# Optimization experiments

Hardware: AMD Instinct MI355X
Metric: run time of the kernel (lower is better)

## Reference

```python
import jax, jax.numpy as jnp
import numpy as np

B_BATCH = 128
IN_F = 1024
OUT_F = 1024
CODE = 2
FACTOR = 1.0


def setup_inputs() -> dict:
    key = jax.random.key(0)
    k = jax.random.split(key, 7)
    bound = 1.0 / np.sqrt(IN_F)
    return {
        "input": jax.random.normal(k[0], (B_BATCH, IN_F), dtype=jnp.float32),
        "codes": jax.random.normal(k[1], (B_BATCH, CODE, CODE), dtype=jnp.float32),
        "weight": jax.random.uniform(k[2], (IN_F, OUT_F), minval=-bound, maxval=bound, dtype=jnp.float32),
        "A": jax.random.uniform(k[3], (IN_F, CODE), minval=-bound, maxval=bound, dtype=jnp.float32),
        "B": jax.random.uniform(k[4], (CODE, OUT_F), minval=-bound, maxval=bound, dtype=jnp.float32),
        "bias": jax.random.uniform(k[5], (OUT_F,), minval=-bound, maxval=bound, dtype=jnp.float32),
        "bias_context": jax.random.uniform(k[6], (CODE, OUT_F), minval=-bound, maxval=bound, dtype=jnp.float32),
    }


def reference(input, codes, weight, A, B, bias, bias_context):
    # per-sample low-rank modulation: A [in,code] x codes [b,code,code] -> [b,in,code]
    w = jnp.einsum('ir,brp->bip', A, codes)
    # [b,in,code] x B [code,out] -> [b,in,out]
    context_weights = jnp.einsum('bir,rj->bij', w, B)
    # diag(codes) [b,code] @ bias_context [code,out] -> [b,out]
    context_bias = jnp.diagonal(codes, axis1=-2, axis2=-1) @ bias_context
    combined_weight = weight + FACTOR * context_weights  # [b,in,out]
    combined_bias = bias + FACTOR * context_bias          # [b,out]
    return jnp.einsum('bi,bij->bj', input, combined_weight) + combined_bias
```

## Files before the change

### kernel.cpp

```cpp
#include <hip/hip_runtime.h>

#define N_BATCH 128
#define IN_F 1024
#define OUT_F 1024
#define BT 8
#define JT 32
#define SEG 32
#define RSTRIDE 36
#define SSTRIDE 292

__global__ __launch_bounds__(256) void geps_one(
    const float* __restrict__ input,
    const float* __restrict__ codes,
    const float* __restrict__ weight,
    const float* __restrict__ A,
    const float* __restrict__ Bm,
    const float* __restrict__ bias,
    const float* __restrict__ bctx,
    float* __restrict__ out)
{
    __shared__ __align__(16) float s[SEG * SSTRIDE];
    __shared__ float s_u[BT][2];
    __shared__ float s_v[BT][4];

    const int t = threadIdx.x;
    const int j0 = blockIdx.x * JT;
    const int b0 = blockIdx.y * BT;

    #pragma unroll
    for (int it = 0; it < 8; ++it) {
        const int F = t + 256 * it;
        const int r = F >> 8;
        const int i4 = F & 255;
        const int ks = i4 >> 3, g = i4 & 7;
        const float4 val = ((const float4*)input)[(size_t)(b0 + r) * (IN_F / 4) + i4];
        *(float4*)&s[ks * SSTRIDE + r * RSTRIDE + 4 * g] = val;
    }
    __syncthreads();

    {
        const int grp = t >> 4, l = t & 15;
        const int row = grp >> 1, rr = grp & 1;
        float p = 0.f;
        #pragma unroll 4
        for (int ii = 0; ii < 64; ++ii) {
            const int i = l + 16 * ii;
            const float x = s[(i >> 5) * SSTRIDE + row * RSTRIDE + (i & 31)];
            p = fmaf(x, A[2 * i + rr], p);
        }
        #pragma unroll
        for (int off = 8; off > 0; off >>= 1)
            p += __shfl_down(p, off, 16);
        if (l == 0) s_u[row][rr] = p;
    }
    __syncthreads();

    if (t < BT) {
        const int b = b0 + t;
        const float u0 = s_u[t][0], u1 = s_u[t][1];
        const float c00 = codes[b * 4 + 0], c01 = codes[b * 4 + 1];
        const float c10 = codes[b * 4 + 2], c11 = codes[b * 4 + 3];
        s_v[t][0] = fmaf(u0, c00, u1 * c10);
        s_v[t][1] = fmaf(u0, c01, u1 * c11);
        s_v[t][2] = c00;
        s_v[t][3] = c11;
    }

    const int jg = t & 7, ks = t >> 3;
    const int col4 = (j0 >> 2) + jg;
    const float4* W4 = (const float4*)weight;
    const float* segbase = &s[ks * SSTRIDE];

    float4 acc[BT];
    #pragma unroll
    for (int r = 0; r < BT; ++r) acc[r] = make_float4(0.f, 0.f, 0.f, 0.f);

    #pragma unroll
    for (int g = 0; g < 8; ++g) {
        float4 a[BT];
        #pragma unroll
        for (int r = 0; r < BT; ++r)
            a[r] = *(const float4*)&segbase[r * RSTRIDE + 4 * g];
        #pragma unroll
        for (int q = 0; q < 4; ++q) {
            const float4 w = W4[(size_t)(ks * 32 + 4 * g + q) * (OUT_F / 4) + col4];
            #pragma unroll
            for (int r = 0; r < BT; ++r) {
                const float av = (q == 0) ? a[r].x : (q == 1) ? a[r].y
                               : (q == 2) ? a[r].z : a[r].w;
                acc[r].x = fmaf(av, w.x, acc[r].x);
                acc[r].y = fmaf(av, w.y, acc[r].y);
                acc[r].z = fmaf(av, w.z, acc[r].z);
                acc[r].w = fmaf(av, w.w, acc[r].w);
            }
        }
    }
    __syncthreads();

    #pragma unroll
    for (int r = 0; r < BT; ++r)
        *(float4*)&s[ks * SSTRIDE + r * RSTRIDE + 4 * jg] = acc[r];
    __syncthreads();

    {
        const int row = t >> 5, col = t & 31;
        float sum = 0.f;
        #pragma unroll
        for (int k = 0; k < SEG; ++k)
            sum += s[k * SSTRIDE + row * RSTRIDE + col];

        const int j = j0 + col;
        const int b = b0 + row;
        const float v0 = s_v[row][0], v1 = s_v[row][1];
        const float c00 = s_v[row][2], c11 = s_v[row][3];
        out[(size_t)b * OUT_F + j] = sum
            + v0 * Bm[j] + v1 * Bm[OUT_F + j]
            + bias[j]
            + c00 * bctx[j] + c11 * bctx[OUT_F + j];
    }
}

extern "C" void kernel_launch(void* const* d_in, const int* in_sizes, int n_in,
                              void* d_out, int out_size, void* d_ws, size_t ws_size,
                              hipStream_t stream) {
    const float* input = (const float*)d_in[0];
    const float* codes = (const float*)d_in[1];
    const float* weight = (const float*)d_in[2];
    const float* A = (const float*)d_in[3];
    const float* Bm = (const float*)d_in[4];
    const float* bias = (const float*)d_in[5];
    const float* bctx = (const float*)d_in[6];
    float* out = (float*)d_out;

    dim3 grid(OUT_F / JT, N_BATCH / BT);
    dim3 block(256);
    geps_one<<<grid, block, 0, stream>>>(input, codes, weight, A, Bm, bias, bctx, out);
}
```

Measured before the change: 77.35 us.

## Software-pipeline weight and LDS loads, hoist epilogue loads, vectorize A reduction

All global loads (input tile, bias/Bm/bctx columns, codes) are issued up front so their latency overlaps. The u = x·A reduction now uses float4 loads of A and x with one 32-lane reduction computing both rank components. The main weight loop double-buffers weight rows two groups ahead and shared-memory activations one group ahead, and launch_bounds is set to request 2 blocks per CU. This aims to hide global and LDS latency in a bandwidth-bound GEMV-like kernel, at the cost of more registers and a risk of spills under the occupancy hint.

```diff
diff --git a/kernel.cpp b/kernel.cpp
--- a/kernel.cpp
+++ b/kernel.cpp
@@ -9,7 +9,7 @@
 #define RSTRIDE 36
 #define SSTRIDE 292
 
-__global__ __launch_bounds__(256) void geps_one(
+__global__ __launch_bounds__(256, 2) void geps_two(
     const float* __restrict__ input,
     const float* __restrict__ codes,
     const float* __restrict__ weight,
@@ -27,39 +27,65 @@
     const int j0 = blockIdx.x * JT;
     const int b0 = blockIdx.y * BT;
 
+    float4 stg[8];
+    #pragma unroll
+    for (int it = 0; it < 8; ++it) {
+        const int F = t + 256 * it;
+        const int r = F >> 8;
+        const int i4 = F & 255;
+        stg[it] = ((const float4*)input)[(size_t)(b0 + r) * (IN_F / 4) + i4];
+    }
+
+    const int jcol = j0 + (t & 31);
+    const float bm0 = Bm[jcol];
+    const float bm1 = Bm[OUT_F + jcol];
+    const float bj  = bias[jcol];
+    const float bq0 = bctx[jcol];
+    const float bq1 = bctx[OUT_F + jcol];
+
+    float c00 = 0.f, c01 = 0.f, c10 = 0.f, c11 = 0.f;
+    if (t < BT) {
+        const int b = b0 + t;
+        c00 = codes[b * 4 + 0]; c01 = codes[b * 4 + 1];
+        c10 = codes[b * 4 + 2]; c11 = codes[b * 4 + 3];
+    }
+
     #pragma unroll
     for (int it = 0; it < 8; ++it) {
         const int F = t + 256 * it;
         const int r = F >> 8;
         const int i4 = F & 255;
         const int ks = i4 >> 3, g = i4 & 7;
-        const float4 val = ((const float4*)input)[(size_t)(b0 + r) * (IN_F / 4) + i4];
-        *(float4*)&s[ks * SSTRIDE + r * RSTRIDE + 4 * g] = val;
+        *(float4*)&s[ks * SSTRIDE + r * RSTRIDE + 4 * g] = stg[it];
     }
     __syncthreads();
 
     {
-        const int grp = t >> 4, l = t & 15;
-        const int row = grp >> 1, rr = grp & 1;
-        float p = 0.f;
-        #pragma unroll 4
-        for (int ii = 0; ii < 64; ++ii) {
-            const int i = l + 16 * ii;
-            const float x = s[(i >> 5) * SSTRIDE + row * RSTRIDE + (i & 31)];
-            p = fmaf(x, A[2 * i + rr], p);
+        const int row = t >> 5, l = t & 31;
+        float u0 = 0.f, u1 = 0.f;
+        #pragma unroll
+        for (int ii = 0; ii < 8; ++ii) {
+            const int i4 = l + 32 * ii;
+            const int ks = i4 >> 3, g = i4 & 7;
+            const float4 x  = *(const float4*)&s[ks * SSTRIDE + row * RSTRIDE + 4 * g];
+            const float4 A0 = ((const float4*)A)[2 * i4];
+            const float4 A1 = ((const float4*)A)[2 * i4 + 1];
+            u0 = fmaf(x.x, A0.x, u0); u1 = fmaf(x.x, A0.y, u1);
+            u0 = fmaf(x.y, A0.z, u0); u1 = fmaf(x.y, A0.w, u1);
+            u0 = fmaf(x.z, A1.x, u0); u1 = fmaf(x.z, A1.y, u1);
+            u0 = fmaf(x.w, A1.z, u0); u1 = fmaf(x.w, A1.w, u1);
         }
         #pragma unroll
-        for (int off = 8; off > 0; off >>= 1)
-            p += __shfl_down(p, off, 16);
-        if (l == 0) s_u[row][rr] = p;
+        for (int off = 16; off > 0; off >>= 1) {
+            u0 += __shfl_down(u0, off, 32);
+            u1 += __shfl_down(u1, off, 32);
+        }
+        if (l == 0) { s_u[row][0] = u0; s_u[row][1] = u1; }
     }
     __syncthreads();
 
     if (t < BT) {
-        const int b = b0 + t;
         const float u0 = s_u[t][0], u1 = s_u[t][1];
-        const float c00 = codes[b * 4 + 0], c01 = codes[b * 4 + 1];
-        const float c10 = codes[b * 4 + 2], c11 = codes[b * 4 + 3];
         s_v[t][0] = fmaf(u0, c00, u1 * c10);
         s_v[t][1] = fmaf(u0, c01, u1 * c11);
         s_v[t][2] = c00;
@@ -68,31 +94,52 @@
 
     const int jg = t & 7, ks = t >> 3;
     const int col4 = (j0 >> 2) + jg;
-    const float4* W4 = (const float4*)weight;
+    const float4* Wc = (const float4*)weight + col4;
     const float* segbase = &s[ks * SSTRIDE];
 
     float4 acc[BT];
     #pragma unroll
     for (int r = 0; r < BT; ++r) acc[r] = make_float4(0.f, 0.f, 0.f, 0.f);
 
+    float4 w0[4], w1[4], aC[BT];
+    #pragma unroll
+    for (int q = 0; q < 4; ++q) w0[q] = Wc[(size_t)(ks * 32 + q) * (OUT_F / 4)];
+    #pragma unroll
+    for (int q = 0; q < 4; ++q) w1[q] = Wc[(size_t)(ks * 32 + 4 + q) * (OUT_F / 4)];
+    #pragma unroll
+    for (int r = 0; r < BT; ++r) aC[r] = *(const float4*)&segbase[r * RSTRIDE];
+
     #pragma unroll
     for (int g = 0; g < 8; ++g) {
-        float4 a[BT];
-        #pragma unroll
-        for (int r = 0; r < BT; ++r)
-            a[r] = *(const float4*)&segbase[r * RSTRIDE + 4 * g];
+        float4 wn[4];
+        if (g < 6) {
+            #pragma unroll
+            for (int q = 0; q < 4; ++q)
+                wn[q] = Wc[(size_t)(ks * 32 + 4 * (g + 2) + q) * (OUT_F / 4)];
+        }
+        float4 aN[BT];
+        if (g < 7) {
+            #pragma unroll
+            for (int r = 0; r < BT; ++r)
+                aN[r] = *(const float4*)&segbase[r * RSTRIDE + 4 * (g + 1)];
+        }
         #pragma unroll
         for (int q = 0; q < 4; ++q) {
-            const float4 w = W4[(size_t)(ks * 32 + 4 * g + q) * (OUT_F / 4) + col4];
             #pragma unroll
             for (int r = 0; r < BT; ++r) {
-                const float av = (q == 0) ? a[r].x : (q == 1) ? a[r].y
-                               : (q == 2) ? a[r].z : a[r].w;
-                acc[r].x = fmaf(av, w.x, acc[r].x);
-                acc[r].y = fmaf(av, w.y, acc[r].y);
-                acc[r].z = fmaf(av, w.z, acc[r].z);
-                acc[r].w = fmaf(av, w.w, acc[r].w);
+                const float av = (q == 0) ? aC[r].x : (q == 1) ? aC[r].y
+                               : (q == 2) ? aC[r].z : aC[r].w;
+                acc[r].x = fmaf(av, w0[q].x, acc[r].x);
+                acc[r].y = fmaf(av, w0[q].y, acc[r].y);
+                acc[r].z = fmaf(av, w0[q].z, acc[r].z);
+                acc[r].w = fmaf(av, w0[q].w, acc[r].w);
             }
+        }
+        if (g < 7) {
+            #pragma unroll
+            for (int q = 0; q < 4; ++q) { w0[q] = w1[q]; w1[q] = wn[q]; }
+            #pragma unroll
+            for (int r = 0; r < BT; ++r) aC[r] = aN[r];
         }
     }
     __syncthreads();
@@ -109,14 +156,12 @@
         for (int k = 0; k < SEG; ++k)
             sum += s[k * SSTRIDE + row * RSTRIDE + col];
 
-        const int j = j0 + col;
-        const int b = b0 + row;
         const float v0 = s_v[row][0], v1 = s_v[row][1];
-        const float c00 = s_v[row][2], c11 = s_v[row][3];
-        out[(size_t)b * OUT_F + j] = sum
-            + v0 * Bm[j] + v1 * Bm[OUT_F + j]
-            + bias[j]
-            + c00 * bctx[j] + c11 * bctx[OUT_F + j];
+        const float k00 = s_v[row][2], k11 = s_v[row][3];
+        out[(size_t)(b0 + row) * OUT_F + jcol] = sum
+            + v0 * bm0 + v1 * bm1
+            + bj
+            + k00 * bq0 + k11 * bq1;
     }
 }
 
@@ -134,5 +179,5 @@
 
     dim3 grid(OUT_F / JT, N_BATCH / BT);
     dim3 block(256);
-    geps_one<<<grid, block, 0, stream>>>(input, codes, weight, A, Bm, bias, bctx, out);
+    geps_two<<<grid, block, 0, stream>>>(input, codes, weight, A, Bm, bias, bctx, out);
 }
```

Result: faster. 73.59 us (-4.9%).
